# Performance work log

Hardware: AMD Instinct MI355X
Metric: run time of the kernel (lower is better)

The kernel has to match this reference:

```python
import jax, jax.numpy as jnp
import numpy as np
import math

B, L, D, H, DK, DFF = 4, 1024, 1024, 16, 64, 4096
NUM_BUCKETS, MAX_DIST = 32, 128


def _relative_position_bucket(rel):
    # bidirectional T5 bucketing; rel = memory_pos - context_pos
    nb = NUM_BUCKETS // 2
    n = -rel
    ret = (n < 0).astype(jnp.int32) * nb
    n = jnp.abs(n)
    max_exact = nb // 2
    is_small = n < max_exact
    val_if_large = max_exact + (
        jnp.log(jnp.maximum(n, 1).astype(jnp.float32) / max_exact)
        / math.log(MAX_DIST / max_exact)
        * (nb - max_exact)
    ).astype(jnp.int32)
    val_if_large = jnp.minimum(val_if_large, nb - 1)
    return ret + jnp.where(is_small, n.astype(jnp.int32), val_if_large)


def t5_layernorm(x, w, eps):
    # no mean subtraction, no bias (T5 style)
    var = jnp.mean(jnp.square(x.astype(jnp.float32)), axis=-1, keepdims=True)
    return w * (x / jnp.sqrt(var + eps))


def setup_inputs() -> dict:
    key = jax.random.key(0)
    ks = jax.random.split(key, 12)
    inp = {
        "src": jax.random.normal(ks[0], (B, L, D), dtype=jnp.float32),
        "enc_position": jnp.broadcast_to(jnp.arange(L, dtype=jnp.int32), (B, L)),
        "ln1_w": jnp.ones((D,), jnp.float32),
        "wq": jax.random.normal(ks[1], (H * DK, D), jnp.float32) * (D * DK) ** -0.5,
        "bq": jnp.zeros((H * DK,), jnp.float32),
        "wk": jax.random.normal(ks[2], (H * DK, D), jnp.float32) * D ** -0.5,
        "bk": jnp.zeros((H * DK,), jnp.float32),
        "wv": jax.random.normal(ks[3], (H * DK, D), jnp.float32) * D ** -0.5,
        "bv": jnp.zeros((H * DK,), jnp.float32),
        "fc_w": jax.random.normal(ks[4], (D, H * DK), jnp.float32) * (H * DK) ** -0.5,
        "fc_b": jnp.zeros((D,), jnp.float32),
        "rel_bias": jax.random.normal(ks[5], (NUM_BUCKETS, H), jnp.float32) * 0.02,
        "ln2_w": jnp.ones((D,), jnp.float32),
        "wi": jax.random.normal(ks[6], (DFF, D), jnp.float32) * D ** -0.5,
        "wo": jax.random.normal(ks[7], (D, DFF), jnp.float32) * DFF ** -0.5,
    }
    return inp


def reference(src, enc_position, ln1_w, wq, bq, wk, bk, wv, bv, fc_w, fc_b,
              rel_bias, ln2_w, wi, wo):
    b, l, d = src.shape
    temp = DK ** 0.5

    # --- Multi-head self attention (pre-LN, T5 relative bias) ---
    proj = t5_layernorm(src, ln1_w, 1e-12)
    q = (proj @ wq.T + bq).reshape(b, l, H, DK).transpose(0, 2, 1, 3)  # [b,h,l,dk]
    k = (proj @ wk.T + bk).reshape(b, l, H, DK).transpose(0, 2, 1, 3)
    v = (proj @ wv.T + bv).reshape(b, l, H, DK).transpose(0, 2, 1, 3)

    # relative position bias: [b, h, l_q, l_k]
    rel = enc_position[:, None, :] - enc_position[:, :, None]  # mem - ctx
    bucket = _relative_position_bucket(rel)                    # [b, l, l]
    position_bias = rel_bias[bucket].transpose(0, 3, 1, 2)     # [b, h, l, l]

    scores = jnp.einsum("bhqd,bhkd->bhqk", q / temp, k) + position_bias
    attn = jax.nn.softmax(scores, axis=-1)                     # dropout = eval no-op
    ctx = jnp.einsum("bhqk,bhkd->bhqd", attn, v)
    ctx = ctx.transpose(0, 2, 1, 3).reshape(b, l, H * DK)
    attn_out = ctx @ fc_w.T + fc_b + src                       # residual
    attn_sum = jnp.sum(attn, axis=1)                           # [b, l, l]

    # --- Position-wise FFN (pre-LN, gelu, no biases) ---
    nx = t5_layernorm(attn_out, ln2_w, 1e-6)
    h = jax.nn.gelu(nx @ wi.T, approximate=False)
    out = attn_out + h @ wo.T
    return out, attn_sum, position_bias
```

## Files before the change

kernel.cpp:

```cpp
#include <hip/hip_runtime.h>
#include <hip/hip_bf16.h>
#include <math.h>

typedef __attribute__((ext_vector_type(8))) short short8;
typedef __attribute__((ext_vector_type(4))) float f32x4;
typedef unsigned short u16;

__device__ __forceinline__ u16 f2bf(float f) {
  union { float f; unsigned u; } x; x.f = f;
  unsigned r = x.u + 0x7fffu + ((x.u >> 16) & 1u);
  return (u16)(r >> 16);
}

__device__ __forceinline__ void gload16(const void* g, void* l) {
  auto gp = reinterpret_cast<const __attribute__((address_space(1))) void*>(
      reinterpret_cast<uintptr_t>(g));
  auto lp = reinterpret_cast<__attribute__((address_space(3))) void*>(
      reinterpret_cast<uintptr_t>(l));
  __builtin_amdgcn_global_load_lds(gp, lp, 16, 0, 0);
}

__device__ __forceinline__ int bucket_fn(int rel) {
  int n = -rel;
  int ret = 0;
  if (n < 0) { ret = 16; n = -n; }
  if (n < 8) return ret + n;
  int e = 31 - __clz(n);
  unsigned nn = (unsigned)n * (unsigned)n;
  int f = 2 * e + ((nn >= (1u << (2 * e + 1))) ? 1 : 0) - 6;
  int val = 8 + f;
  if (val > 15) val = 15;
  return ret + val;
}

__global__ __launch_bounds__(256) void prep(
    const float* __restrict__ wq, const float* __restrict__ wk,
    const float* __restrict__ wv, const float* __restrict__ fcw,
    const float* __restrict__ wi, const float* __restrict__ wo,
    const float* __restrict__ bq, const float* __restrict__ bk,
    const float* __restrict__ bv, const float* __restrict__ rel_bias,
    u16* __restrict__ wqb, u16* __restrict__ wkb, u16* __restrict__ wvb,
    u16* __restrict__ fcwb, u16* __restrict__ wib, u16* __restrict__ wob,
    float* __restrict__ fb, float* __restrict__ tab) {
  const int blk = blockIdx.x, t = threadIdx.x;
  if (blk < 12288) {
    const float* s; u16* d; int rel;
    if (blk < 1024)      { s = wq;  d = wqb;  rel = blk; }
    else if (blk < 2048) { s = wk;  d = wkb;  rel = blk - 1024; }
    else if (blk < 3072) { s = wv;  d = wvb;  rel = blk - 2048; }
    else if (blk < 4096) { s = fcw; d = fcwb; rel = blk - 3072; }
    else if (blk < 8192) { s = wi;  d = wib;  rel = blk - 4096; }
    else                 { s = wo;  d = wob;  rel = blk - 8192; }
    const int i = (rel * 256 + t) * 4;
    float4 v = *(const float4*)&s[i];
    d[i + 0] = f2bf(v.x); d[i + 1] = f2bf(v.y);
    d[i + 2] = f2bf(v.z); d[i + 3] = f2bf(v.w);
  } else if (blk < 12300) {
    const int i = (blk - 12288) * 256 + t;
    fb[i] = i < 1024 ? bq[i] : (i < 2048 ? bk[i - 1024] : bv[i - 2048]);
  } else {
    const int idx = (blk - 12300) * 256 + t;
    const int h = idx >> 11;
    const int rel = (idx & 2047) - 1024;
    tab[idx] = rel_bias[bucket_fn(rel) * 16 + h];
  }
}

__global__ __launch_bounds__(256) void write_pb(const float* __restrict__ tab,
                                                float* __restrict__ pb) {
  const int i = blockIdx.x, h = blockIdx.y, t = threadIdx.x;
  __shared__ float tabs[2048];
  ((float4*)tabs)[t]       = ((const float4*)(tab + h * 2048))[t];
  ((float4*)tabs)[t + 256] = ((const float4*)(tab + h * 2048))[t + 256];
  __syncthreads();
  const int j = t * 4;
  float4 o;
  o.x = tabs[j + 0 - i + 1024];
  o.y = tabs[j + 1 - i + 1024];
  o.z = tabs[j + 2 - i + 1024];
  o.w = tabs[j + 3 - i + 1024];
#pragma unroll
  for (int b = 0; b < 4; b++)
    *(float4*)&pb[(((size_t)(b * 16 + h)) * 1024 + i) * 1024 + j] = o;
}

__global__ __launch_bounds__(256) void t5_ln(const float* __restrict__ x,
                                             const float* __restrict__ wgt,
                                             float eps, u16* __restrict__ out) {
  const int row = blockIdx.x, t = threadIdx.x;
  const float4 v = ((const float4*)(x + (size_t)row * 1024))[t];
  float ss = v.x * v.x + v.y * v.y + v.z * v.z + v.w * v.w;
#pragma unroll
  for (int off = 1; off < 64; off <<= 1) ss += __shfl_xor(ss, off, 64);
  __shared__ float red[4];
  if ((t & 63) == 0) red[t >> 6] = ss;
  __syncthreads();
  float tot = red[0] + red[1] + red[2] + red[3];
  float inv = 1.0f / sqrtf(tot * (1.0f / 1024.0f) + eps);
  const float4 wv = ((const float4*)wgt)[t];
  u16* o = out + (size_t)row * 1024 + t * 4;
  o[0] = f2bf(v.x * inv * wv.x);
  o[1] = f2bf(v.y * inv * wv.y);
  o[2] = f2bf(v.z * inv * wv.z);
  o[3] = f2bf(v.w * inv * wv.w);
}

__global__ __launch_bounds__(256) void transpose_v(const u16* __restrict__ v,
                                                   u16* __restrict__ vt) {
  __shared__ u16 T[64][72];
  const int bh = blockIdx.y;
  const int l0 = blockIdx.x * 64;
  const int t = threadIdx.x;
  const int sr = t >> 3, sc = (t & 7) * 8;
  const u16* vb = v + (size_t)bh * 65536;
  *(short8*)&T[sr][sc]      = *(const short8*)&vb[(size_t)(l0 + sr) * 64 + sc];
  *(short8*)&T[sr + 32][sc] = *(const short8*)&vb[(size_t)(l0 + sr + 32) * 64 + sc];
  __syncthreads();
  u16* vtb = vt + (size_t)bh * 65536;
  short8 o0, o1;
#pragma unroll
  for (int u = 0; u < 8; u++) {
    ((u16*)&o0)[u] = T[sc + u][sr];
    ((u16*)&o1)[u] = T[sc + u][sr + 32];
  }
  *(short8*)&vtb[(size_t)sr * 1024 + l0 + sc]        = o0;
  *(short8*)&vtb[(size_t)(sr + 32) * 1024 + l0 + sc] = o1;
}

template<int MODE>
__global__ __launch_bounds__(256, 3) void gemm_nt(
    const u16* __restrict__ A, const u16* __restrict__ Bw,
    int M, int N, int K,
    const float* __restrict__ bias, const float* __restrict__ res,
    float scale, float* __restrict__ outF, u16* __restrict__ outB) {
  __shared__ u16 As[3][4096];
  __shared__ u16 Bs[3][4096];
  const int t = threadIdx.x;
  const int w = t >> 6, lane = t & 63;
  const int wr = w >> 1, wc = w & 1;
  const int g = lane >> 4, lc = lane & 15;
  const int m0 = blockIdx.y * 128, n0 = blockIdx.x * 128;

  const int srow = w * 16 + (lane >> 2);
  const int sc8  = (lane & 3) ^ ((srow >> 1) & 3);
  const u16* Ag = &A[(size_t)(m0 + srow) * K + sc8 * 8];
  const u16* Bg = &Bw[(size_t)(n0 + srow) * K + sc8 * 8];
  const size_t row64 = (size_t)64 * K;
  const int swz = (lc >> 1) & 3;

  const int NT = K >> 5;
  f32x4 acc[4][4] = {};

  auto stage = [&](int buf, int tt) {
    const int k0 = tt << 5;
    u16* lA = &As[buf][w * 512];
    u16* lB = &Bs[buf][w * 512];
    gload16(Ag + k0, lA);
    gload16(Ag + row64 + k0, lA + 2048);
    gload16(Bg + k0, lB);
    gload16(Bg + row64 + k0, lB + 2048);
  };

  stage(0, 0);
  stage(1, 1);

  for (int tt = 0; tt < NT; tt++) {
    const int cur = tt % 3;
    if (tt < NT - 1) {
      asm volatile("s_waitcnt vmcnt(4)" ::: "memory");
    } else {
      asm volatile("s_waitcnt vmcnt(0)" ::: "memory");
    }
    __builtin_amdgcn_s_barrier();
    short8 af[4], bf[4];
#pragma unroll
    for (int mi = 0; mi < 4; mi++)
      af[mi] = *(short8*)&As[cur][(wr * 64 + mi * 16 + lc) * 32 + (g ^ swz) * 8];
#pragma unroll
    for (int ni = 0; ni < 4; ni++)
      bf[ni] = *(short8*)&Bs[cur][(wc * 64 + ni * 16 + lc) * 32 + (g ^ swz) * 8];
    if (tt + 2 < NT) stage((tt + 2) % 3, tt + 2);
#pragma unroll
    for (int mi = 0; mi < 4; mi++)
#pragma unroll
      for (int ni = 0; ni < 4; ni++)
        acc[mi][ni] = __builtin_amdgcn_mfma_f32_16x16x32_bf16(af[mi], bf[ni], acc[mi][ni], 0, 0, 0);
  }

#pragma unroll
  for (int mi = 0; mi < 4; mi++) {
#pragma unroll
    for (int ni = 0; ni < 4; ni++) {
#pragma unroll
      for (int r = 0; r < 4; r++) {
        const int row = m0 + wr * 64 + mi * 16 + g * 4 + r;
        const int col = n0 + wc * 64 + ni * 16 + lc;
        float v = acc[mi][ni][r];
        if (MODE == 0) {
          const int which = col >> 10, c = col & 1023;
          v = (v + bias[col]) * (which == 0 ? scale : 1.0f);
          const int b = row >> 10, pos = row & 1023, hh = c >> 6, dk = c & 63;
          outB[(size_t)which * 4194304 +
               (((size_t)(b * 16 + hh)) * 1024 + pos) * 64 + dk] = f2bf(v);
        } else {
          v = 0.5f * v * (1.0f + erff(v * 0.70710678118654752440f));
          outB[(size_t)row * (size_t)N + col] = f2bf(v);
        }
      }
    }
  }
}

template<int MODE>
__global__ __launch_bounds__(256, 4) void gemm_nt64(
    const u16* __restrict__ A, const u16* __restrict__ Bw,
    int M, int N, int K,
    const float* __restrict__ bias, const float* __restrict__ res,
    float* __restrict__ outF) {
  __shared__ u16 As[3][2048];
  __shared__ u16 Bs[3][4096];
  const int t = threadIdx.x;
  const int w = t >> 6, lane = t & 63;
  const int wr = w >> 1, wc = w & 1;
  const int g = lane >> 4, lc = lane & 15;
  const int m0 = blockIdx.y * 64, n0 = blockIdx.x * 128;

  const int srow = w * 16 + (lane >> 2);
  const int sc8  = (lane & 3) ^ ((srow >> 1) & 3);
  const u16* Ag = &A[(size_t)(m0 + srow) * K + sc8 * 8];
  const u16* Bg = &Bw[(size_t)(n0 + srow) * K + sc8 * 8];
  const size_t row64 = (size_t)64 * K;
  const int swz = (lc >> 1) & 3;

  const int NT = K >> 5;
  f32x4 acc[2][4] = {};

  auto stage = [&](int buf, int tt) {
    const int k0 = tt << 5;
    gload16(Ag + k0, &As[buf][w * 512]);
    gload16(Bg + k0, &Bs[buf][w * 512]);
    gload16(Bg + row64 + k0, &Bs[buf][w * 512 + 2048]);
  };

  stage(0, 0);
  stage(1, 1);

  for (int tt = 0; tt < NT; tt++) {
    const int cur = tt % 3;
    if (tt < NT - 1) {
      asm volatile("s_waitcnt vmcnt(3)" ::: "memory");
    } else {
      asm volatile("s_waitcnt vmcnt(0)" ::: "memory");
    }
    __builtin_amdgcn_s_barrier();
    short8 af[2], bf[4];
#pragma unroll
    for (int mi = 0; mi < 2; mi++)
      af[mi] = *(short8*)&As[cur][(wr * 32 + mi * 16 + lc) * 32 + (g ^ swz) * 8];
#pragma unroll
    for (int ni = 0; ni < 4; ni++)
      bf[ni] = *(short8*)&Bs[cur][(wc * 64 + ni * 16 + lc) * 32 + (g ^ swz) * 8];
    if (tt + 2 < NT) stage((tt + 2) % 3, tt + 2);
#pragma unroll
    for (int mi = 0; mi < 2; mi++)
#pragma unroll
      for (int ni = 0; ni < 4; ni++)
        acc[mi][ni] = __builtin_amdgcn_mfma_f32_16x16x32_bf16(af[mi], bf[ni], acc[mi][ni], 0, 0, 0);
  }

#pragma unroll
  for (int mi = 0; mi < 2; mi++) {
#pragma unroll
    for (int ni = 0; ni < 4; ni++) {
#pragma unroll
      for (int r = 0; r < 4; r++) {
        const int row = m0 + wr * 32 + mi * 16 + g * 4 + r;
        const int col = n0 + wc * 64 + ni * 16 + lc;
        float v = acc[mi][ni][r];
        if (MODE == 1) {
          v += bias[col] + res[(size_t)row * 1024 + col];
        } else {
          v += res[(size_t)row * 1024 + col];
        }
        outF[(size_t)row * 1024 + col] = v;
      }
    }
  }
}

__global__ __launch_bounds__(256) void attn_kernel(
    const u16* __restrict__ q, const u16* __restrict__ k,
    const u16* __restrict__ vt, const float* __restrict__ tab,
    u16* __restrict__ ctx, float* __restrict__ ml) {
  const int bh = blockIdx.y;
  const int h = bh & 15, b = bh >> 4;
  const int i0 = blockIdx.x * 64;
  const int t = threadIdx.x, w = t >> 6, lane = t & 63;
  const int g = lane >> 4, lc = lane & 15;
  const int sr = t >> 3;
  const int swc = ((t & 7) ^ (sr & 7)) * 8;
  const int sc = (t & 7) * 8;

  __shared__ u16 Ks[2][64][64];
  __shared__ u16 Vts[2][64][64];
  __shared__ u16 P[4][16][64];
  __shared__ float tabs[2048];

  const u16* qb  = q + (size_t)bh * 65536;
  const u16* kb  = k + (size_t)bh * 65536;
  const u16* vtb = vt + (size_t)bh * 65536;

  ((float4*)tabs)[t]       = ((const float4*)(tab + h * 2048))[t];
  ((float4*)tabs)[t + 256] = ((const float4*)(tab + h * 2048))[t + 256];

  const short8 aq0 = *(const short8*)&qb[(size_t)(i0 + w * 16 + lc) * 64 + g * 8];
  const short8 aq1 = *(const short8*)&qb[(size_t)(i0 + w * 16 + lc) * 64 + 32 + g * 8];

  {
    short8 ka = *(const short8*)&kb[(size_t)sr * 64 + sc];
    short8 kc = *(const short8*)&kb[(size_t)(sr + 32) * 64 + sc];
    short8 va = *(const short8*)&vtb[(size_t)sr * 1024 + sc];
    short8 vc = *(const short8*)&vtb[(size_t)(sr + 32) * 1024 + sc];
    *(short8*)&Ks[0][sr][swc]       = ka;
    *(short8*)&Ks[0][sr + 32][swc]  = kc;
    *(short8*)&Vts[0][sr][swc]      = va;
    *(short8*)&Vts[0][sr + 32][swc] = vc;
  }
  __syncthreads();

  const int rx = lc & 7;
  const int ibase = 1024 - i0 - (w * 16 + g * 4) + lc;

  float m_r[4] = {-INFINITY, -INFINITY, -INFINITY, -INFINITY};
  float l_r[4] = {0.f, 0.f, 0.f, 0.f};
  f32x4 cacc[4] = {};

  for (int tt = 0; tt < 16; tt++) {
    const int buf = tt & 1;
    const int j0 = tt * 64;

    short8 nka, nkc, nva, nvc;
    if (tt < 15) {
      const int jn = j0 + 64;
      nka = *(const short8*)&kb[(size_t)(jn + sr) * 64 + sc];
      nkc = *(const short8*)&kb[(size_t)(jn + sr + 32) * 64 + sc];
      nva = *(const short8*)&vtb[(size_t)sr * 1024 + jn + sc];
      nvc = *(const short8*)&vtb[(size_t)(sr + 32) * 1024 + jn + sc];
    }

    f32x4 s[4] = {};
#pragma unroll
    for (int ni = 0; ni < 4; ni++) {
      short8 b0 = *(short8*)&Ks[buf][ni * 16 + lc][(g ^ rx) * 8];
      short8 b1 = *(short8*)&Ks[buf][ni * 16 + lc][((4 + g) ^ rx) * 8];
      s[ni] = __builtin_amdgcn_mfma_f32_16x16x32_bf16(aq0, b0, s[ni], 0, 0, 0);
      s[ni] = __builtin_amdgcn_mfma_f32_16x16x32_bf16(aq1, b1, s[ni], 0, 0, 0);
    }
#pragma unroll
    for (int ni = 0; ni < 4; ni++)
#pragma unroll
      for (int r = 0; r < 4; r++)
        s[ni][r] += tabs[ibase + j0 + ni * 16 - r];

#pragma unroll
    for (int r = 0; r < 4; r++) {
      float tm = fmaxf(fmaxf(s[0][r], s[1][r]), fmaxf(s[2][r], s[3][r]));
#pragma unroll
      for (int off = 1; off < 16; off <<= 1) tm = fmaxf(tm, __shfl_xor(tm, off, 64));
      const float mn = fmaxf(m_r[r], tm);
      const float scl = expf(m_r[r] - mn);
      float rs = 0.f;
#pragma unroll
      for (int ni = 0; ni < 4; ni++) {
        float p = expf(s[ni][r] - mn);
        s[ni][r] = p;
        rs += p;
      }
#pragma unroll
      for (int off = 1; off < 16; off <<= 1) rs += __shfl_xor(rs, off, 64);
      l_r[r] = l_r[r] * scl + rs;
      m_r[r] = mn;
#pragma unroll
      for (int d = 0; d < 4; d++) cacc[d][r] *= scl;
    }

#pragma unroll
    for (int ni = 0; ni < 4; ni++)
#pragma unroll
      for (int r = 0; r < 4; r++) {
        const int prow = g * 4 + r;
        P[w][prow][(((ni * 2 + (lc >> 3)) ^ (prow & 7)) << 3) | (lc & 7)] = f2bf(s[ni][r]);
      }

    short8 ap0 = *(short8*)&P[w][lc][(g ^ rx) * 8];
    short8 ap1 = *(short8*)&P[w][lc][((4 + g) ^ rx) * 8];
#pragma unroll
    for (int d = 0; d < 4; d++) {
      short8 bv0 = *(short8*)&Vts[buf][d * 16 + lc][(g ^ rx) * 8];
      short8 bv1 = *(short8*)&Vts[buf][d * 16 + lc][((4 + g) ^ rx) * 8];
      cacc[d] = __builtin_amdgcn_mfma_f32_16x16x32_bf16(ap0, bv0, cacc[d], 0, 0, 0);
      cacc[d] = __builtin_amdgcn_mfma_f32_16x16x32_bf16(ap1, bv1, cacc[d], 0, 0, 0);
    }

    if (tt < 15) {
      *(short8*)&Ks[buf ^ 1][sr][swc]       = nka;
      *(short8*)&Ks[buf ^ 1][sr + 32][swc]  = nkc;
      *(short8*)&Vts[buf ^ 1][sr][swc]      = nva;
      *(short8*)&Vts[buf ^ 1][sr + 32][swc] = nvc;
    }
    __syncthreads();
  }

  float inv[4];
#pragma unroll
  for (int r = 0; r < 4; r++) inv[r] = 1.0f / l_r[r];
#pragma unroll
  for (int d = 0; d < 4; d++)
#pragma unroll
    for (int r = 0; r < 4; r++) {
      const int pos = i0 + w * 16 + g * 4 + r;
      ctx[((size_t)b * 1024 + pos) * 1024 + h * 64 + d * 16 + lc] = f2bf(cacc[d][r] * inv[r]);
    }
  if (lc == 0) {
#pragma unroll
    for (int r = 0; r < 4; r++) {
      const int i = i0 + w * 16 + g * 4 + r;
      ml[(size_t)bh * 1024 + i] = m_r[r];
      ml[65536 + (size_t)bh * 1024 + i] = l_r[r];
    }
  }
}

__global__ __launch_bounds__(256) void attn_sum_kernel(
    const u16* __restrict__ q, const u16* __restrict__ k,
    const float* __restrict__ tab, const float* __restrict__ ml,
    float* __restrict__ asum) {
  const int b = blockIdx.z;
  const int i0 = blockIdx.y * 64;
  const int j0 = blockIdx.x * 64;
  const int t = threadIdx.x, w = t >> 6, lane = t & 63;
  const int g = lane >> 4, lc = lane & 15;
  const int sr = t >> 3;
  const int swc = ((t & 7) ^ (sr & 7)) * 8;
  const int sc = (t & 7) * 8;
  const int rx = lc & 7;
  __shared__ u16 Ks[64][64];
  __shared__ float tabs[128];

  f32x4 acc[4] = {};

  for (int h = 0; h < 16; h++) {
    const int bh = b * 16 + h;
    __syncthreads();
    const u16* kb = k + (size_t)bh * 65536;
    *(short8*)&Ks[sr][swc]      = *(const short8*)&kb[(size_t)(j0 + sr) * 64 + sc];
    *(short8*)&Ks[sr + 32][swc] = *(const short8*)&kb[(size_t)(j0 + sr + 32) * 64 + sc];
    if (t < 127) tabs[t] = tab[h * 2048 + (j0 - i0 - 63 + t) + 1024];
    __syncthreads();
    const u16* qb = q + (size_t)bh * 65536;
    short8 aq0 = *(const short8*)&qb[(size_t)(i0 + w * 16 + lc) * 64 + g * 8];
    short8 aq1 = *(const short8*)&qb[(size_t)(i0 + w * 16 + lc) * 64 + 32 + g * 8];
    f32x4 s[4] = {};
#pragma unroll
    for (int ni = 0; ni < 4; ni++) {
      short8 b0 = *(short8*)&Ks[ni * 16 + lc][(g ^ rx) * 8];
      short8 b1 = *(short8*)&Ks[ni * 16 + lc][((4 + g) ^ rx) * 8];
      s[ni] = __builtin_amdgcn_mfma_f32_16x16x32_bf16(aq0, b0, s[ni], 0, 0, 0);
      s[ni] = __builtin_amdgcn_mfma_f32_16x16x32_bf16(aq1, b1, s[ni], 0, 0, 0);
    }
    float mm[4], li[4];
#pragma unroll
    for (int r = 0; r < 4; r++) {
      const int i = i0 + w * 16 + g * 4 + r;
      mm[r] = ml[(size_t)bh * 1024 + i];
      li[r] = 1.0f / ml[65536 + (size_t)bh * 1024 + i];
    }
#pragma unroll
    for (int ni = 0; ni < 4; ni++)
#pragma unroll
      for (int r = 0; r < 4; r++) {
        float sv = s[ni][r] + tabs[ni * 16 + lc - w * 16 - g * 4 - r + 63];
        acc[ni][r] += expf(sv - mm[r]) * li[r];
      }
  }
#pragma unroll
  for (int ni = 0; ni < 4; ni++)
#pragma unroll
    for (int r = 0; r < 4; r++) {
      const int i = i0 + w * 16 + g * 4 + r;
      asum[((size_t)b * 1024 + i) * 1024 + j0 + ni * 16 + lc] = acc[ni][r];
    }
}

extern "C" void kernel_launch(void* const* d_in, const int* in_sizes, int n_in,
                              void* d_out, int out_size, void* d_ws, size_t ws_size,
                              hipStream_t stream) {
  const float* src      = (const float*)d_in[0];
  const float* ln1_w    = (const float*)d_in[2];
  const float* wq       = (const float*)d_in[3];
  const float* bq       = (const float*)d_in[4];
  const float* wk       = (const float*)d_in[5];
  const float* bk       = (const float*)d_in[6];
  const float* wv       = (const float*)d_in[7];
  const float* bv       = (const float*)d_in[8];
  const float* fc_w     = (const float*)d_in[9];
  const float* fc_b     = (const float*)d_in[10];
  const float* rel_bias = (const float*)d_in[11];
  const float* ln2_w    = (const float*)d_in[12];
  const float* wi       = (const float*)d_in[13];
  const float* wo       = (const float*)d_in[14];

  const size_t MB = 1u << 20;
  char* ws = (char*)d_ws;
  u16* wq_b   = (u16*)(ws + 0 * MB);
  u16* wk_b   = (u16*)(ws + 2 * MB);
  u16* wv_b   = (u16*)(ws + 4 * MB);
  u16* fcw_b  = (u16*)(ws + 6 * MB);
  u16* wi_b   = (u16*)(ws + 8 * MB);
  u16* wo_b   = (u16*)(ws + 16 * MB);
  u16* proj_b = (u16*)(ws + 24 * MB);
  u16* q_b    = (u16*)(ws + 32 * MB);
  u16* k_b    = (u16*)(ws + 40 * MB);
  u16* v_b    = (u16*)(ws + 48 * MB);
  u16* vt_b   = (u16*)(ws + 56 * MB);
  u16* h_b    = (u16*)(ws + 32 * MB);
  u16* ctx_b  = (u16*)(ws + 64 * MB);
  float* attn_out = (float*)(ws + 72 * MB);
  float* ml   = (float*)(ws + 88 * MB);
  float* tab  = (float*)(ws + 88 * MB + 512 * 1024);
  float* fb   = (float*)(ws + 90 * MB);

  float* outF = (float*)d_out;
  float* asum = outF + 4194304;
  float* pb   = outF + 8388608;

  prep<<<12428, 256, 0, stream>>>(wq, wk, wv, fc_w, wi, wo, bq, bk, bv, rel_bias,
                                  wq_b, wk_b, wv_b, fcw_b, wi_b, wo_b, fb, tab);

  write_pb<<<dim3(1024, 16), 256, 0, stream>>>(tab, pb);

  t5_ln<<<4096, 256, 0, stream>>>(src, ln1_w, 1e-12f, proj_b);

  gemm_nt<0><<<dim3(24, 32), 256, 0, stream>>>(proj_b, wq_b, 4096, 3072, 1024, fb, nullptr, 0.125f, nullptr, q_b);

  transpose_v<<<dim3(16, 64), 256, 0, stream>>>(v_b, vt_b);
  attn_kernel<<<dim3(16, 64), 256, 0, stream>>>(q_b, k_b, vt_b, tab, ctx_b, ml);
  attn_sum_kernel<<<dim3(16, 16, 4), 256, 0, stream>>>(q_b, k_b, tab, ml, asum);

  gemm_nt64<1><<<dim3(8, 64), 256, 0, stream>>>(ctx_b, fcw_b, 4096, 1024, 1024, fc_b, src, attn_out);

  t5_ln<<<4096, 256, 0, stream>>>(attn_out, ln2_w, 1e-6f, proj_b);

  gemm_nt<2><<<dim3(32, 32), 256, 0, stream>>>(proj_b, wi_b, 4096, 4096, 1024, nullptr, nullptr, 1.0f, nullptr, h_b);
  gemm_nt64<3><<<dim3(8, 64), 256, 0, stream>>>(h_b, wo_b, 4096, 1024, 4096, nullptr, attn_out, outF);
}
```

Measured before the change: 395.7 us.

## Use base-2 exponent softmax and stage GEMM epilogue through LDS for vector stores

```diff
diff --git a/kernel.cpp b/kernel.cpp
--- a/kernel.cpp
+++ b/kernel.cpp
@@ -5,6 +5,8 @@
 typedef __attribute__((ext_vector_type(8))) short short8;
 typedef __attribute__((ext_vector_type(4))) float f32x4;
 typedef unsigned short u16;
+
+#define L2E 1.44269504088896340736f
 
 __device__ __forceinline__ u16 f2bf(float f) {
   union { float f; unsigned u; } x; x.f = f;
@@ -187,27 +189,48 @@
         acc[mi][ni] = __builtin_amdgcn_mfma_f32_16x16x32_bf16(af[mi], bf[ni], acc[mi][ni], 0, 0, 0);
   }
 
+  u16* Es = &As[0][0];
+  __syncthreads();
 #pragma unroll
   for (int mi = 0; mi < 4; mi++) {
 #pragma unroll
     for (int ni = 0; ni < 4; ni++) {
 #pragma unroll
       for (int r = 0; r < 4; r++) {
-        const int row = m0 + wr * 64 + mi * 16 + g * 4 + r;
         const int col = n0 + wc * 64 + ni * 16 + lc;
         float v = acc[mi][ni][r];
         if (MODE == 0) {
-          const int which = col >> 10, c = col & 1023;
-          v = (v + bias[col]) * (which == 0 ? scale : 1.0f);
-          const int b = row >> 10, pos = row & 1023, hh = c >> 6, dk = c & 63;
-          outB[(size_t)which * 4194304 +
-               (((size_t)(b * 16 + hh)) * 1024 + pos) * 64 + dk] = f2bf(v);
+          v = (v + bias[col]) * ((col >> 10) == 0 ? scale : 1.0f);
         } else {
           v = 0.5f * v * (1.0f + erff(v * 0.70710678118654752440f));
-          outB[(size_t)row * (size_t)N + col] = f2bf(v);
         }
+        Es[wr * 2048 + (g * 4 + r) * 128 + wc * 64 + ni * 16 + lc] = f2bf(v);
       }
     }
+    __syncthreads();
+    {
+      const int rr = t >> 3;
+      const int wr2 = rr >> 4, r16 = rr & 15;
+      const int cc = (t & 7) * 16;
+      short8 o0 = *(short8*)&Es[wr2 * 2048 + r16 * 128 + cc];
+      short8 o1 = *(short8*)&Es[wr2 * 2048 + r16 * 128 + cc + 8];
+      const int row = m0 + wr2 * 64 + mi * 16 + r16;
+      if (MODE == 0) {
+        const int col0 = n0 + cc;
+        const int which = col0 >> 10, c = col0 & 1023;
+        const int hh = c >> 6, dk = c & 63;
+        const int b = row >> 10, pos = row & 1023;
+        u16* dst = outB + (size_t)which * 4194304 +
+                   (((size_t)(b * 16 + hh)) * 1024 + pos) * 64 + dk;
+        *(short8*)dst = o0;
+        *(short8*)(dst + 8) = o1;
+      } else {
+        u16* dst = outB + (size_t)row * (size_t)N + n0 + cc;
+        *(short8*)dst = o0;
+        *(short8*)(dst + 8) = o1;
+      }
+    }
+    __syncthreads();
   }
 }
 
@@ -310,8 +333,14 @@
   const u16* kb  = k + (size_t)bh * 65536;
   const u16* vtb = vt + (size_t)bh * 65536;
 
-  ((float4*)tabs)[t]       = ((const float4*)(tab + h * 2048))[t];
-  ((float4*)tabs)[t + 256] = ((const float4*)(tab + h * 2048))[t + 256];
+  {
+    float4 t0 = ((const float4*)(tab + h * 2048))[t];
+    float4 t1 = ((const float4*)(tab + h * 2048))[t + 256];
+    t0.x *= L2E; t0.y *= L2E; t0.z *= L2E; t0.w *= L2E;
+    t1.x *= L2E; t1.y *= L2E; t1.z *= L2E; t1.w *= L2E;
+    ((float4*)tabs)[t]       = t0;
+    ((float4*)tabs)[t + 256] = t1;
+  }
 
   const short8 aq0 = *(const short8*)&qb[(size_t)(i0 + w * 16 + lc) * 64 + g * 8];
   const short8 aq1 = *(const short8*)&qb[(size_t)(i0 + w * 16 + lc) * 64 + 32 + g * 8];
@@ -368,11 +397,11 @@
 #pragma unroll
       for (int off = 1; off < 16; off <<= 1) tm = fmaxf(tm, __shfl_xor(tm, off, 64));
       const float mn = fmaxf(m_r[r], tm);
-      const float scl = expf(m_r[r] - mn);
+      const float scl = __builtin_amdgcn_exp2f(m_r[r] - mn);
       float rs = 0.f;
 #pragma unroll
       for (int ni = 0; ni < 4; ni++) {
-        float p = expf(s[ni][r] - mn);
+        float p = __builtin_amdgcn_exp2f(s[ni][r] - mn);
         s[ni][r] = p;
         rs += p;
       }
@@ -455,7 +484,7 @@
     const u16* kb = k + (size_t)bh * 65536;
     *(short8*)&Ks[sr][swc]      = *(const short8*)&kb[(size_t)(j0 + sr) * 64 + sc];
     *(short8*)&Ks[sr + 32][swc] = *(const short8*)&kb[(size_t)(j0 + sr + 32) * 64 + sc];
-    if (t < 127) tabs[t] = tab[h * 2048 + (j0 - i0 - 63 + t) + 1024];
+    if (t < 127) tabs[t] = tab[h * 2048 + (j0 - i0 - 63 + t) + 1024] * L2E;
     __syncthreads();
     const u16* qb = q + (size_t)bh * 65536;
     short8 aq0 = *(const short8*)&qb[(size_t)(i0 + w * 16 + lc) * 64 + g * 8];
@@ -480,7 +509,7 @@
 #pragma unroll
       for (int r = 0; r < 4; r++) {
         float sv = s[ni][r] + tabs[ni * 16 + lc - w * 16 - g * 4 - r + 63];
-        acc[ni][r] += expf(sv - mm[r]) * li[r];
+        acc[ni][r] += __builtin_amdgcn_exp2f(sv - mm[r]) * li[r];
       }
   }
 #pragma unroll
@@ -541,7 +570,8 @@
 
   t5_ln<<<4096, 256, 0, stream>>>(src, ln1_w, 1e-12f, proj_b);
 
-  gemm_nt<0><<<dim3(24, 32), 256, 0, stream>>>(proj_b, wq_b, 4096, 3072, 1024, fb, nullptr, 0.125f, nullptr, q_b);
+  gemm_nt<0><<<dim3(24, 32), 256, 0, stream>>>(proj_b, wq_b, 4096, 3072, 1024, fb, nullptr,
+                                               0.125f * L2E, nullptr, q_b);
 
   transpose_v<<<dim3(16, 64), 256, 0, stream>>>(v_b, vt_b);
   attn_kernel<<<dim3(16, 64), 256, 0, stream>>>(q_b, k_b, vt_b, tab, ctx_b, ml);
```

Result: faster. 366.3 us (-7.4%).
